# Kernel tuning notes

Hardware: AMD Instinct MI355X
Metric: run time of the kernel (lower is better)

The kernel has to match this reference:

```python
import jax, jax.numpy as jnp
import numpy as np


def setup_inputs() -> dict:
    key = jax.random.key(0)
    ks = jax.random.split(key, 8)
    n_src, n_dst, n_edges = 100000, 50000, 600000
    d_in, d_out = 128, 128
    n_reuse, n_cache = 5000, 8000
    full_dst_len = n_dst + n_reuse

    feat_src = jax.random.normal(ks[0], (n_src, d_in), jnp.float32)
    src = jax.random.randint(ks[1], (n_edges,), 0, n_src)
    dst = jax.random.randint(ks[2], (n_edges,), 0, n_dst)
    # xavier-ish init for the two bias-free Linear layers (stored as [out, in] like torch)
    W_self = jax.random.normal(ks[3], (d_out, d_in), jnp.float32) / np.sqrt(d_in).astype(np.float32)
    W_neigh = jax.random.normal(ks[4], (d_out, d_in), jnp.float32) / np.sqrt(d_in).astype(np.float32)
    # reuse_indices must be unique positions within [0, full_dst_len)
    reuse_indices = jnp.sort(jax.random.permutation(ks[5], full_dst_len)[:n_reuse])
    reuse_embedding = jax.random.normal(ks[6], (n_reuse, d_out), jnp.float32)
    cache_indices = jax.random.randint(ks[7], (n_cache,), 0, full_dst_len)
    return dict(feat_src=feat_src, W_self=W_self, W_neigh=W_neigh,
                reuse_embedding=reuse_embedding, src=src, dst=dst,
                reuse_indices=reuse_indices, cache_indices=cache_indices,
                n_dst=n_dst)


def reference(feat_src, W_self, W_neigh, reuse_embedding, src, dst,
              reuse_indices, cache_indices, n_dst):
    # --- GraphSAGE 'mean' aggregation on a block graph ---
    feat_dst = feat_src[:n_dst]                         # [n_dst, D_in]
    msgs = feat_src[src]                                # [E, D_in] copy_src gather
    ssum = jax.ops.segment_sum(msgs, dst, num_segments=n_dst)          # [n_dst, D_in]
    deg = jax.ops.segment_sum(jnp.ones_like(msgs[:, 0]), dst, num_segments=n_dst)
    h_neigh = jnp.where(deg[:, None] > 0, ssum / jnp.maximum(deg, 1.0)[:, None], 0.0)
    rst = feat_dst @ W_self.T + h_neigh @ W_neigh.T     # fc_self + fc_neigh

    # --- cache-reuse scatter merge (flag == 0 path) ---
    n_reuse = reuse_indices.shape[0]
    full_dst_len = n_dst + n_reuse
    keep = jnp.ones((full_dst_len,), dtype=bool).at[reuse_indices].set(False)
    unprune_indices = jnp.nonzero(keep, size=n_dst)[0]  # np.delete equivalent
    full = jnp.zeros((full_dst_len, rst.shape[1]), rst.dtype)
    full = full.at[unprune_indices].set(rst).at[reuse_indices].set(reuse_embedding)
    cache_embedding = jax.lax.stop_gradient(full[cache_indices])  # .detach()
    return full, cache_embedding
```

## Files before the change

### kernel.cpp

```cpp
#include <hip/hip_runtime.h>

#define N_SRC   100000
#define N_DST   50000
#define D       128
#define MAXDEG  64

typedef __attribute__((ext_vector_type(8))) short bf16x8;
typedef __attribute__((ext_vector_type(4))) float f32x4;

__device__ __forceinline__ unsigned short f2bf(float f) {
    unsigned u = __float_as_uint(f);
    u += 0x7FFFu + ((u >> 16) & 1u);
    return (unsigned short)(u >> 16);
}
__device__ __forceinline__ float bf2f(unsigned short u) {
    return __uint_as_float((unsigned)u << 16);
}

__global__ void build_ell_kernel(const int* __restrict__ src,
                                 const int* __restrict__ dst,
                                 int* __restrict__ ell,
                                 int* __restrict__ cnt,
                                 int n_edges) {
    int e = blockIdx.x * blockDim.x + threadIdx.x;
    if (e >= n_edges) return;
    int d = dst[e];
    int pos = atomicAdd(&cnt[d], 1);
    if (pos < MAXDEG)
        ell[(size_t)d * MAXDEG + pos] = src[e];
}

__global__ void aux_kernel(const int* __restrict__ reuse_idx,
                           int* __restrict__ rowpos, int n_reuse,
                           const float* __restrict__ Wself,
                           const float* __restrict__ Wneigh,
                           unsigned short* __restrict__ wbf) {
    int i = blockIdx.x * blockDim.x + threadIdx.x;
    if (i < 128 * 256) {
        int n = i >> 8;
        int k = i & 255;
        float v = (k < 128) ? Wself[n * 128 + k] : Wneigh[n * 128 + (k - 128)];
        wbf[i] = f2bf(v);
    }
    if (i < N_DST) {
        int lo = 0, hi = n_reuse;
        while (lo < hi) {
            int mid = (lo + hi) >> 1;
            if (reuse_idx[mid] - mid > i) hi = mid; else lo = mid + 1;
        }
        rowpos[i] = i + lo;
    }
}

__global__ __launch_bounds__(256)
void featconv_kernel(const float* __restrict__ feat,
                     unsigned int* __restrict__ featbf_u32,
                     int n4) {
    int stride = gridDim.x * blockDim.x;
    for (int i = blockIdx.x * blockDim.x + threadIdx.x; i < n4; i += stride) {
        float4 v = *(const float4*)(feat + (size_t)i * 4);
        uint2 o;
        o.x = (unsigned)f2bf(v.x) | ((unsigned)f2bf(v.y) << 16);
        o.y = (unsigned)f2bf(v.z) | ((unsigned)f2bf(v.w) << 16);
        *(uint2*)(featbf_u32 + (size_t)i * 2) = o;
    }
}

__global__ __launch_bounds__(256)
void gather_bf16_kernel(const unsigned short* __restrict__ featbf,
                        const int* __restrict__ ell,
                        const int* __restrict__ cnt,
                        uint4* __restrict__ hneigh_u4) {
    int gid  = blockIdx.x * blockDim.x + threadIdx.x;
    int row  = gid >> 4;
    int lane = gid & 15;
    if (row >= N_DST) return;

    int deg = cnt[row];
    int n = min(deg, MAXDEG);
    float inv = 1.0f / fmaxf((float)deg, 1.0f);
    const int* rell = ell + (size_t)row * MAXDEG;

    float acc[8];
#pragma unroll
    for (int k = 0; k < 8; ++k) acc[k] = 0.f;

    union U { uint4 v; unsigned short us[8]; };
    int j = 0;
    for (; j + 4 <= n; j += 4) {
        int s0 = rell[j + 0];
        int s1 = rell[j + 1];
        int s2 = rell[j + 2];
        int s3 = rell[j + 3];
        U a, b, c, d;
        a.v = *(const uint4*)(featbf + (size_t)s0 * D + lane * 8);
        b.v = *(const uint4*)(featbf + (size_t)s1 * D + lane * 8);
        c.v = *(const uint4*)(featbf + (size_t)s2 * D + lane * 8);
        d.v = *(const uint4*)(featbf + (size_t)s3 * D + lane * 8);
#pragma unroll
        for (int k = 0; k < 8; ++k)
            acc[k] += (bf2f(a.us[k]) + bf2f(b.us[k])) + (bf2f(c.us[k]) + bf2f(d.us[k]));
    }
    for (; j < n; ++j) {
        int s = rell[j];
        U a;
        a.v = *(const uint4*)(featbf + (size_t)s * D + lane * 8);
#pragma unroll
        for (int k = 0; k < 8; ++k) acc[k] += bf2f(a.us[k]);
    }
    uint4 o;
    o.x = (unsigned)f2bf(acc[0] * inv) | ((unsigned)f2bf(acc[1] * inv) << 16);
    o.y = (unsigned)f2bf(acc[2] * inv) | ((unsigned)f2bf(acc[3] * inv) << 16);
    o.z = (unsigned)f2bf(acc[4] * inv) | ((unsigned)f2bf(acc[5] * inv) << 16);
    o.w = (unsigned)f2bf(acc[6] * inv) | ((unsigned)f2bf(acc[7] * inv) << 16);
    hneigh_u4[(size_t)row * 16 + lane] = o;
}

__global__ __launch_bounds__(256)
void gather_kernel(const float* __restrict__ feat,
                   const int* __restrict__ ell,
                   const int* __restrict__ cnt,
                   unsigned int* __restrict__ hneigh_u32) {
    int gid  = blockIdx.x * blockDim.x + threadIdx.x;
    int row  = gid >> 5;
    int lane = gid & 31;
    if (row >= N_DST) return;

    int deg = cnt[row];
    int n = min(deg, MAXDEG);
    float inv = 1.0f / fmaxf((float)deg, 1.0f);
    const int* rell = ell + (size_t)row * MAXDEG;

    float4 acc = make_float4(0.f, 0.f, 0.f, 0.f);
    int j = 0;
    for (; j + 4 <= n; j += 4) {
        int s0 = rell[j + 0];
        int s1 = rell[j + 1];
        int s2 = rell[j + 2];
        int s3 = rell[j + 3];
        float4 v0 = *(const float4*)&feat[(size_t)s0 * D + 4 * lane];
        float4 v1 = *(const float4*)&feat[(size_t)s1 * D + 4 * lane];
        float4 v2 = *(const float4*)&feat[(size_t)s2 * D + 4 * lane];
        float4 v3 = *(const float4*)&feat[(size_t)s3 * D + 4 * lane];
        acc.x += v0.x + v1.x + v2.x + v3.x;
        acc.y += v0.y + v1.y + v2.y + v3.y;
        acc.z += v0.z + v1.z + v2.z + v3.z;
        acc.w += v0.w + v1.w + v2.w + v3.w;
    }
    for (; j < n; ++j) {
        int s = rell[j];
        float4 v = *(const float4*)&feat[(size_t)s * D + 4 * lane];
        acc.x += v.x;
        acc.y += v.y;
        acc.z += v.z;
        acc.w += v.w;
    }
    unsigned p0 = (unsigned)f2bf(acc.x * inv) | ((unsigned)f2bf(acc.y * inv) << 16);
    unsigned p1 = (unsigned)f2bf(acc.z * inv) | ((unsigned)f2bf(acc.w * inv) << 16);
    uint2 out; out.x = p0; out.y = p1;
    *(uint2*)&hneigh_u32[(size_t)row * 64 + 2 * lane] = out;
}

__global__ __launch_bounds__(256, 2)
void gemm_kernel(const float* __restrict__ feat,
                 const unsigned short* __restrict__ hneigh,
                 const unsigned short* __restrict__ wbf,
                 const int* __restrict__ rowpos,
                 float* __restrict__ full) {
    __shared__ unsigned short Wl[128 * 256];

    int tid = threadIdx.x;
    {
        int n = tid >> 1;
        int ckbase = (tid & 1) * 16;
        const uint4* s = (const uint4*)(wbf + n * 256);
        uint4* d = (uint4*)(Wl + n * 256);
#pragma unroll
        for (int i = 0; i < 16; ++i) {
            int ck = ckbase + i;
            d[ck ^ (n & 7)] = s[ck];
        }
    }
    __syncthreads();

    int wv   = tid >> 6;
    int lane = tid & 63;
    int l15  = lane & 15;
    int q    = lane >> 4;
    int rowbase = blockIdx.x * 128 + wv * 32;

    f32x4 acc[2][8];
#pragma unroll
    for (int rt = 0; rt < 2; ++rt)
#pragma unroll
        for (int ct = 0; ct < 8; ++ct) acc[rt][ct] = (f32x4){0.f, 0.f, 0.f, 0.f};

    int r0c = min(rowbase + l15,      N_DST - 1);
    int r1c = min(rowbase + 16 + l15, N_DST - 1);

#pragma unroll 1
    for (int s = 0; s < 4; ++s) {
        int k0 = s * 32 + q * 8;
        float4 a0lo = *(const float4*)(feat + (size_t)r0c * D + k0);
        float4 a0hi = *(const float4*)(feat + (size_t)r0c * D + k0 + 4);
        float4 a1lo = *(const float4*)(feat + (size_t)r1c * D + k0);
        float4 a1hi = *(const float4*)(feat + (size_t)r1c * D + k0 + 4);
        union { bf16x8 v; unsigned short u[8]; } a0, a1;
        a0.u[0] = f2bf(a0lo.x); a0.u[1] = f2bf(a0lo.y);
        a0.u[2] = f2bf(a0lo.z); a0.u[3] = f2bf(a0lo.w);
        a0.u[4] = f2bf(a0hi.x); a0.u[5] = f2bf(a0hi.y);
        a0.u[6] = f2bf(a0hi.z); a0.u[7] = f2bf(a0hi.w);
        a1.u[0] = f2bf(a1lo.x); a1.u[1] = f2bf(a1lo.y);
        a1.u[2] = f2bf(a1lo.z); a1.u[3] = f2bf(a1lo.w);
        a1.u[4] = f2bf(a1hi.x); a1.u[5] = f2bf(a1hi.y);
        a1.u[6] = f2bf(a1hi.z); a1.u[7] = f2bf(a1hi.w);
#pragma unroll
        for (int ct = 0; ct < 8; ++ct) {
            int n = ct * 16 + l15;
            int ck = s * 4 + q;
            bf16x8 b = *(const bf16x8*)(Wl + n * 256 + ((ck ^ (n & 7)) << 3));
            acc[0][ct] = __builtin_amdgcn_mfma_f32_16x16x32_bf16(a0.v, b, acc[0][ct], 0, 0, 0);
            acc[1][ct] = __builtin_amdgcn_mfma_f32_16x16x32_bf16(a1.v, b, acc[1][ct], 0, 0, 0);
        }
    }
#pragma unroll 1
    for (int s = 0; s < 4; ++s) {
        int k0 = s * 32 + q * 8;
        bf16x8 a0 = *(const bf16x8*)(hneigh + (size_t)r0c * D + k0);
        bf16x8 a1 = *(const bf16x8*)(hneigh + (size_t)r1c * D + k0);
#pragma unroll
        for (int ct = 0; ct < 8; ++ct) {
            int n = ct * 16 + l15;
            int ck = 16 + s * 4 + q;
            bf16x8 b = *(const bf16x8*)(Wl + n * 256 + ((ck ^ (n & 7)) << 3));
            acc[0][ct] = __builtin_amdgcn_mfma_f32_16x16x32_bf16(a0, b, acc[0][ct], 0, 0, 0);
            acc[1][ct] = __builtin_amdgcn_mfma_f32_16x16x32_bf16(a1, b, acc[1][ct], 0, 0, 0);
        }
    }

#pragma unroll
    for (int rt = 0; rt < 2; ++rt) {
#pragma unroll
        for (int reg = 0; reg < 4; ++reg) {
            int gm = rowbase + rt * 16 + q * 4 + reg;
            if (gm < N_DST) {
                int jj = rowpos[gm];
                float* outr = full + (size_t)jj * D + l15;
#pragma unroll
                for (int ct = 0; ct < 8; ++ct)
                    outr[ct * 16] = acc[rt][ct][reg];
            }
        }
    }
}

__global__ void reuse_copy_kernel(const float* __restrict__ emb,
                                  const int* __restrict__ ridx,
                                  float* __restrict__ full, int n) {
    int idx = blockIdx.x * blockDim.x + threadIdx.x;
    int r = idx >> 5;
    if (r >= n) return;
    int c4 = (idx & 31) * 4;
    *(float4*)&full[ridx[r] * D + c4] = *(const float4*)&emb[r * D + c4];
}

__global__ void cache_gather_kernel(const float* __restrict__ full,
                                    const int* __restrict__ cidx,
                                    float* __restrict__ out, int n) {
    int idx = blockIdx.x * blockDim.x + threadIdx.x;
    int r = idx >> 5;
    if (r >= n) return;
    int c4 = (idx & 31) * 4;
    *(float4*)&out[r * D + c4] = *(const float4*)&full[cidx[r] * D + c4];
}

extern "C" void kernel_launch(void* const* d_in, const int* in_sizes, int n_in,
                              void* d_out, int out_size, void* d_ws, size_t ws_size,
                              hipStream_t stream) {
    const float* feat_src  = (const float*)d_in[0];
    const float* W_self    = (const float*)d_in[1];
    const float* W_neigh   = (const float*)d_in[2];
    const float* reuse_emb = (const float*)d_in[3];
    const int*   src       = (const int*)d_in[4];
    const int*   dst       = (const int*)d_in[5];
    const int*   reuse_idx = (const int*)d_in[6];
    const int*   cache_idx = (const int*)d_in[7];

    int n_edges = in_sizes[4];
    int n_reuse = in_sizes[6];
    int n_cache = in_sizes[7];
    int full_len = N_DST + n_reuse;

    float* full = (float*)d_out;
    float* cache_out = full + (size_t)full_len * D;

    size_t hneigh_b = (size_t)N_DST * D * sizeof(unsigned short);
    size_t ell_b    = (size_t)N_DST * MAXDEG * sizeof(int);
    size_t need     = hneigh_b + ell_b + 2 * (size_t)N_DST * 4 + 128 * 256 * 2;

    if (ws_size >= need) {
        unsigned short* hneigh = (unsigned short*)d_ws;
        int*   ell    = (int*)((char*)d_ws + hneigh_b);
        int*   cnt    = (int*)((char*)ell + ell_b);
        int*   rowpos = cnt + N_DST;
        unsigned short* wbf = (unsigned short*)(rowpos + N_DST);
        unsigned short* featbf = (unsigned short*)full;

        hipMemsetAsync(cnt, 0, (size_t)N_DST * sizeof(int), stream);

        build_ell_kernel<<<(n_edges + 255) / 256, 256, 0, stream>>>(
            src, dst, ell, cnt, n_edges);

        aux_kernel<<<(N_DST + 255) / 256, 256, 0, stream>>>(
            reuse_idx, rowpos, n_reuse, W_self, W_neigh, wbf);

        featconv_kernel<<<2048, 256, 0, stream>>>(
            feat_src, (unsigned int*)featbf, N_SRC * (D / 4));

        gather_bf16_kernel<<<(N_DST * 16 + 255) / 256, 256, 0, stream>>>(
            featbf, ell, cnt, (uint4*)hneigh);

        gemm_kernel<<<(N_DST + 127) / 128, 256, 0, stream>>>(
            feat_src, hneigh, wbf, rowpos, full);

        reuse_copy_kernel<<<(n_reuse * 32 + 255) / 256, 256, 0, stream>>>(
            reuse_emb, reuse_idx, full, n_reuse);

        cache_gather_kernel<<<(n_cache * 32 + 255) / 256, 256, 0, stream>>>(
            full, cache_idx, cache_out, n_cache);
    } else {
        unsigned short* hneigh = (unsigned short*)d_ws;
        int*   cnt    = (int*)(hneigh + (size_t)N_DST * D);
        int*   rowpos = cnt + N_DST;
        unsigned short* wbf = (unsigned short*)(rowpos + N_DST);
        int* ell = (int*)full;

        hipMemsetAsync(cnt, 0, (size_t)N_DST * sizeof(int), stream);

        build_ell_kernel<<<(n_edges + 255) / 256, 256, 0, stream>>>(
            src, dst, ell, cnt, n_edges);

        aux_kernel<<<(N_DST + 255) / 256, 256, 0, stream>>>(
            reuse_idx, rowpos, n_reuse, W_self, W_neigh, wbf);

        gather_kernel<<<(N_DST * 32 + 255) / 256, 256, 0, stream>>>(
            feat_src, ell, cnt, (unsigned int*)hneigh);

        gemm_kernel<<<(N_DST + 127) / 128, 256, 0, stream>>>(
            feat_src, hneigh, wbf, rowpos, full);

        reuse_copy_kernel<<<(n_reuse * 32 + 255) / 256, 256, 0, stream>>>(
            reuse_emb, reuse_idx, full, n_reuse);

        cache_gather_kernel<<<(n_cache * 32 + 255) / 256, 256, 0, stream>>>(
            full, cache_idx, cache_out, n_cache);
    }
}
```

Baseline: 193.6 us.

## Fuse prep kernels, keep bf16 features in workspace, merge epilogue launches

Folds the count memset, weight conversion, row-position search and fp32-to-bf16 feature conversion into one prep kernel. The bf16 feature copy now lives in workspace and the ELL table lives in the output buffer, and the GEMM reads bf16 self features instead of fp32. The reuse scatter and cache gather become a single epilogue launch. The cache gather binary-searches reuse indices so it does not depend on the reuse writes, which removes an ordering dependency. The aim is fewer launches and less GEMM input traffic, at the cost of extra bf16 rounding on the self-feature path.

```diff
diff --git a/kernel.cpp b/kernel.cpp
--- a/kernel.cpp
+++ b/kernel.cpp
@@ -30,34 +30,34 @@
         ell[(size_t)d * MAXDEG + pos] = src[e];
 }
 
-__global__ void aux_kernel(const int* __restrict__ reuse_idx,
-                           int* __restrict__ rowpos, int n_reuse,
-                           const float* __restrict__ Wself,
-                           const float* __restrict__ Wneigh,
-                           unsigned short* __restrict__ wbf) {
-    int i = blockIdx.x * blockDim.x + threadIdx.x;
-    if (i < 128 * 256) {
-        int n = i >> 8;
-        int k = i & 255;
-        float v = (k < 128) ? Wself[n * 128 + k] : Wneigh[n * 128 + (k - 128)];
-        wbf[i] = f2bf(v);
-    }
-    if (i < N_DST) {
+__global__ __launch_bounds__(256)
+void prep_kernel(const int* __restrict__ reuse_idx,
+                 int* __restrict__ rowpos, int n_reuse,
+                 const float* __restrict__ Wself,
+                 const float* __restrict__ Wneigh,
+                 unsigned short* __restrict__ wbf,
+                 const float* __restrict__ feat,
+                 unsigned int* __restrict__ featbf_u32,
+                 int* __restrict__ cnt) {
+    int tid = blockIdx.x * blockDim.x + threadIdx.x;
+    if (tid < N_DST) {
+        cnt[tid] = 0;
         int lo = 0, hi = n_reuse;
         while (lo < hi) {
             int mid = (lo + hi) >> 1;
-            if (reuse_idx[mid] - mid > i) hi = mid; else lo = mid + 1;
-        }
-        rowpos[i] = i + lo;
-    }
-}
-
-__global__ __launch_bounds__(256)
-void featconv_kernel(const float* __restrict__ feat,
-                     unsigned int* __restrict__ featbf_u32,
-                     int n4) {
+            if (reuse_idx[mid] - mid > tid) hi = mid; else lo = mid + 1;
+        }
+        rowpos[tid] = tid + lo;
+    }
+    if (tid < 128 * 256) {
+        int n = tid >> 8;
+        int k = tid & 255;
+        float v = (k < 128) ? Wself[n * 128 + k] : Wneigh[n * 128 + (k - 128)];
+        wbf[tid] = f2bf(v);
+    }
+    const int n4 = N_SRC * (D / 4);
     int stride = gridDim.x * blockDim.x;
-    for (int i = blockIdx.x * blockDim.x + threadIdx.x; i < n4; i += stride) {
+    for (int i = tid; i < n4; i += stride) {
         float4 v = *(const float4*)(feat + (size_t)i * 4);
         uint2 o;
         o.x = (unsigned)f2bf(v.x) | ((unsigned)f2bf(v.y) << 16);
@@ -116,57 +116,81 @@
     hneigh_u4[(size_t)row * 16 + lane] = o;
 }
 
-__global__ __launch_bounds__(256)
-void gather_kernel(const float* __restrict__ feat,
-                   const int* __restrict__ ell,
-                   const int* __restrict__ cnt,
-                   unsigned int* __restrict__ hneigh_u32) {
-    int gid  = blockIdx.x * blockDim.x + threadIdx.x;
-    int row  = gid >> 5;
-    int lane = gid & 31;
-    if (row >= N_DST) return;
-
-    int deg = cnt[row];
-    int n = min(deg, MAXDEG);
-    float inv = 1.0f / fmaxf((float)deg, 1.0f);
-    const int* rell = ell + (size_t)row * MAXDEG;
-
-    float4 acc = make_float4(0.f, 0.f, 0.f, 0.f);
-    int j = 0;
-    for (; j + 4 <= n; j += 4) {
-        int s0 = rell[j + 0];
-        int s1 = rell[j + 1];
-        int s2 = rell[j + 2];
-        int s3 = rell[j + 3];
-        float4 v0 = *(const float4*)&feat[(size_t)s0 * D + 4 * lane];
-        float4 v1 = *(const float4*)&feat[(size_t)s1 * D + 4 * lane];
-        float4 v2 = *(const float4*)&feat[(size_t)s2 * D + 4 * lane];
-        float4 v3 = *(const float4*)&feat[(size_t)s3 * D + 4 * lane];
-        acc.x += v0.x + v1.x + v2.x + v3.x;
-        acc.y += v0.y + v1.y + v2.y + v3.y;
-        acc.z += v0.z + v1.z + v2.z + v3.z;
-        acc.w += v0.w + v1.w + v2.w + v3.w;
-    }
-    for (; j < n; ++j) {
-        int s = rell[j];
-        float4 v = *(const float4*)&feat[(size_t)s * D + 4 * lane];
-        acc.x += v.x;
-        acc.y += v.y;
-        acc.z += v.z;
-        acc.w += v.w;
-    }
-    unsigned p0 = (unsigned)f2bf(acc.x * inv) | ((unsigned)f2bf(acc.y * inv) << 16);
-    unsigned p1 = (unsigned)f2bf(acc.z * inv) | ((unsigned)f2bf(acc.w * inv) << 16);
-    uint2 out; out.x = p0; out.y = p1;
-    *(uint2*)&hneigh_u32[(size_t)row * 64 + 2 * lane] = out;
-}
-
 __global__ __launch_bounds__(256, 2)
-void gemm_kernel(const float* __restrict__ feat,
+void gemm_kernel(const unsigned short* __restrict__ featbf,
                  const unsigned short* __restrict__ hneigh,
                  const unsigned short* __restrict__ wbf,
                  const int* __restrict__ rowpos,
                  float* __restrict__ full) {
+    __shared__ unsigned short Wl[128 * 256];
+
+    int tid = threadIdx.x;
+    {
+        int n = tid >> 1;
+        int ckbase = (tid & 1) * 16;
+        const uint4* s = (const uint4*)(wbf + n * 256);
+        uint4* d = (uint4*)(Wl + n * 256);
+#pragma unroll
+        for (int i = 0; i < 16; ++i) {
+            int ck = ckbase + i;
+            d[ck ^ (n & 7)] = s[ck];
+        }
+    }
+    __syncthreads();
+
+    int wv   = tid >> 6;
+    int lane = tid & 63;
+    int l15  = lane & 15;
+    int q    = lane >> 4;
+    int rowbase = blockIdx.x * 128 + wv * 32;
+
+    f32x4 acc[2][8];
+#pragma unroll
+    for (int rt = 0; rt < 2; ++rt)
+#pragma unroll
+        for (int ct = 0; ct < 8; ++ct) acc[rt][ct] = (f32x4){0.f, 0.f, 0.f, 0.f};
+
+    int r0c = min(rowbase + l15,      N_DST - 1);
+    int r1c = min(rowbase + 16 + l15, N_DST - 1);
+
+#pragma unroll
+    for (int s = 0; s < 8; ++s) {
+        const unsigned short* A = (s < 4) ? featbf : hneigh;
+        int k0 = (s & 3) * 32 + q * 8;
+        bf16x8 a0 = *(const bf16x8*)(A + (size_t)r0c * D + k0);
+        bf16x8 a1 = *(const bf16x8*)(A + (size_t)r1c * D + k0);
+#pragma unroll
+        for (int ct = 0; ct < 8; ++ct) {
+            int n = ct * 16 + l15;
+            int ck = s * 4 + q;
+            bf16x8 b = *(const bf16x8*)(Wl + n * 256 + ((ck ^ (n & 7)) << 3));
+            acc[0][ct] = __builtin_amdgcn_mfma_f32_16x16x32_bf16(a0, b, acc[0][ct], 0, 0, 0);
+            acc[1][ct] = __builtin_amdgcn_mfma_f32_16x16x32_bf16(a1, b, acc[1][ct], 0, 0, 0);
+        }
+    }
+
+#pragma unroll
+    for (int rt = 0; rt < 2; ++rt) {
+#pragma unroll
+        for (int reg = 0; reg < 4; ++reg) {
+            int gm = rowbase + rt * 16 + q * 4 + reg;
+            if (gm < N_DST) {
+                int jj = rowpos[gm];
+                float* outr = full + (size_t)jj * D + l15;
+#pragma unroll
+                for (int ct = 0; ct < 8; ++ct)
+                    outr[ct * 16] = acc[rt][ct][reg];
+            }
+        }
+    }
+}
+
+__global__ __launch_bounds__(256, 2)
+void gemm_f32a_kernel(const float* __restrict__ feat,
+                      const unsigned short* __restrict__ hneigh,
+                      const unsigned short* __restrict__ wbf,
+                      const int* __restrict__ rowpos,
+                      float* __restrict__ full) {
     __shared__ unsigned short Wl[128 * 256];
 
     int tid = threadIdx.x;
@@ -254,24 +278,31 @@
     }
 }
 
-__global__ void reuse_copy_kernel(const float* __restrict__ emb,
-                                  const int* __restrict__ ridx,
-                                  float* __restrict__ full, int n) {
+__global__ __launch_bounds__(256)
+void epilogue_kernel(const float* __restrict__ emb,
+                     const int* __restrict__ ridx, int n_reuse,
+                     float* __restrict__ full,
+                     const int* __restrict__ cidx,
+                     float* __restrict__ cache_out, int n_cache) {
     int idx = blockIdx.x * blockDim.x + threadIdx.x;
-    int r = idx >> 5;
-    if (r >= n) return;
+    int row = idx >> 5;
     int c4 = (idx & 31) * 4;
-    *(float4*)&full[ridx[r] * D + c4] = *(const float4*)&emb[r * D + c4];
-}
-
-__global__ void cache_gather_kernel(const float* __restrict__ full,
-                                    const int* __restrict__ cidx,
-                                    float* __restrict__ out, int n) {
-    int idx = blockIdx.x * blockDim.x + threadIdx.x;
-    int r = idx >> 5;
-    if (r >= n) return;
-    int c4 = (idx & 31) * 4;
-    *(float4*)&out[r * D + c4] = *(const float4*)&full[cidx[r] * D + c4];
+    if (row < n_reuse) {
+        *(float4*)&full[(size_t)ridx[row] * D + c4] =
+            *(const float4*)&emb[(size_t)row * D + c4];
+    } else if (row < n_reuse + n_cache) {
+        int r = row - n_reuse;
+        int v = cidx[r];
+        int lo = 0, hi = n_reuse;
+        while (lo < hi) {
+            int mid = (lo + hi) >> 1;
+            if (ridx[mid] < v) lo = mid + 1; else hi = mid;
+        }
+        const float* srcp = (lo < n_reuse && ridx[lo] == v)
+            ? emb + (size_t)lo * D
+            : full + (size_t)v * D;
+        *(float4*)&cache_out[(size_t)r * D + c4] = *(const float4*)&srcp[c4];
+    }
 }
 
 extern "C" void kernel_launch(void* const* d_in, const int* in_sizes, int n_in,
@@ -295,10 +326,37 @@
     float* cache_out = full + (size_t)full_len * D;
 
     size_t hneigh_b = (size_t)N_DST * D * sizeof(unsigned short);
+    size_t featbf_b = (size_t)N_SRC * D * sizeof(unsigned short);
     size_t ell_b    = (size_t)N_DST * MAXDEG * sizeof(int);
-    size_t need     = hneigh_b + ell_b + 2 * (size_t)N_DST * 4 + 128 * 256 * 2;
-
-    if (ws_size >= need) {
+    size_t small_b  = 2 * (size_t)N_DST * 4 + 128 * 256 * 2;
+    size_t need_fast = hneigh_b + featbf_b + small_b;
+
+    int ep_rows = n_reuse + n_cache;
+
+    if (ws_size >= need_fast) {
+        unsigned short* hneigh = (unsigned short*)d_ws;
+        unsigned short* featbf = (unsigned short*)((char*)d_ws + hneigh_b);
+        int*   cnt    = (int*)((char*)featbf + featbf_b);
+        int*   rowpos = cnt + N_DST;
+        unsigned short* wbf = (unsigned short*)(rowpos + N_DST);
+        int* ell = (int*)full;
+
+        prep_kernel<<<2048, 256, 0, stream>>>(
+            reuse_idx, rowpos, n_reuse, W_self, W_neigh, wbf,
+            feat_src, (unsigned int*)featbf, cnt);
+
+        build_ell_kernel<<<(n_edges + 255) / 256, 256, 0, stream>>>(
+            src, dst, ell, cnt, n_edges);
+
+        gather_bf16_kernel<<<(N_DST * 16 + 255) / 256, 256, 0, stream>>>(
+            featbf, ell, cnt, (uint4*)hneigh);
+
+        gemm_kernel<<<(N_DST + 127) / 128, 256, 0, stream>>>(
+            featbf, hneigh, wbf, rowpos, full);
+
+        epilogue_kernel<<<(ep_rows * 32 + 255) / 256, 256, 0, stream>>>(
+            reuse_emb, reuse_idx, n_reuse, full, cache_idx, cache_out, n_cache);
+    } else {
         unsigned short* hneigh = (unsigned short*)d_ws;
         int*   ell    = (int*)((char*)d_ws + hneigh_b);
         int*   cnt    = (int*)((char*)ell + ell_b);
@@ -306,53 +364,20 @@
         unsigned short* wbf = (unsigned short*)(rowpos + N_DST);
         unsigned short* featbf = (unsigned short*)full;
 
-        hipMemsetAsync(cnt, 0, (size_t)N_DST * sizeof(int), stream);
+        prep_kernel<<<2048, 256, 0, stream>>>(
+            reuse_idx, rowpos, n_reuse, W_self, W_neigh, wbf,
+            feat_src, (unsigned int*)featbf, cnt);
 
         build_ell_kernel<<<(n_edges + 255) / 256, 256, 0, stream>>>(
             src, dst, ell, cnt, n_edges);
 
-        aux_kernel<<<(N_DST + 255) / 256, 256, 0, stream>>>(
-            reuse_idx, rowpos, n_reuse, W_self, W_neigh, wbf);
-
-        featconv_kernel<<<2048, 256, 0, stream>>>(
-            feat_src, (unsigned int*)featbf, N_SRC * (D / 4));
-
         gather_bf16_kernel<<<(N_DST * 16 + 255) / 256, 256, 0, stream>>>(
             featbf, ell, cnt, (uint4*)hneigh);
 
-        gemm_kernel<<<(N_DST + 127) / 128, 256, 0, stream>>>(
+        gemm_f32a_kernel<<<(N_DST + 127) / 128, 256, 0, stream>>>(
             feat_src, hneigh, wbf, rowpos, full);
 
-        reuse_copy_kernel<<<(n_reuse * 32 + 255) / 256, 256, 0, stream>>>(
-            reuse_emb, reuse_idx, full, n_reuse);
-
-        cache_gather_kernel<<<(n_cache * 32 + 255) / 256, 256, 0, stream>>>(
-            full, cache_idx, cache_out, n_cache);
-    } else {
-        unsigned short* hneigh = (unsigned short*)d_ws;
-        int*   cnt    = (int*)(hneigh + (size_t)N_DST * D);
-        int*   rowpos = cnt + N_DST;
-        unsigned short* wbf = (unsigned short*)(rowpos + N_DST);
-        int* ell = (int*)full;
-
-        hipMemsetAsync(cnt, 0, (size_t)N_DST * sizeof(int), stream);
-
-        build_ell_kernel<<<(n_edges + 255) / 256, 256, 0, stream>>>(
-            src, dst, ell, cnt, n_edges);
-
-        aux_kernel<<<(N_DST + 255) / 256, 256, 0, stream>>>(
-            reuse_idx, rowpos, n_reuse, W_self, W_neigh, wbf);
-
-        gather_kernel<<<(N_DST * 32 + 255) / 256, 256, 0, stream>>>(
-            feat_src, ell, cnt, (unsigned int*)hneigh);
-
-        gemm_kernel<<<(N_DST + 127) / 128, 256, 0, stream>>>(
-            feat_src, hneigh, wbf, rowpos, full);
-
-        reuse_copy_kernel<<<(n_reuse * 32 + 255) / 256, 256, 0, stream>>>(
-            reuse_emb, reuse_idx, full, n_reuse);
-
-        cache_gather_kernel<<<(n_cache * 32 + 255) / 256, 256, 0, stream>>>(
-            full, cache_idx, cache_out, n_cache);
-    }
-}
+        epilogue_kernel<<<(ep_rows * 32 + 255) / 256, 256, 0, stream>>>(
+            reuse_emb, reuse_idx, n_reuse, full, cache_idx, cache_out, n_cache);
+    }
+}
```

After: 191.6 us. About the same (-1.0%).
